# Performance work log

Measured on AMD Instinct MI355X. Metric: run time of the kernel, lower is better.

The kernel has to match this reference:

```python
import jax, jax.numpy as jnp
import numpy as np

BEAM = 10; MAX_LEN = 32; PAD = 1; BOS = 2; EOS = 3
NEG = jnp.float32(-1e30)


def lstm_cell(x, h, c, Wih, Whh, bih, bhh):
    # PyTorch LSTMCell gate order: i, f, g, o
    gates = x @ Wih.T + bih + h @ Whh.T + bhh
    i, f, g, o = jnp.split(gates, 4, axis=-1)
    c2 = jax.nn.sigmoid(f) * c + jax.nn.sigmoid(i) * jnp.tanh(g)
    h2 = jax.nn.sigmoid(o) * jnp.tanh(c2)
    return h2, c2


def setup_inputs() -> dict:
    key = jax.random.key(0)
    ks = jax.random.split(key, 14)
    G, P, E, H, S = 1000, 50000, 500, 500, 32
    s = lambda k, shape: jax.random.normal(k, shape, jnp.float32) * 0.05
    return {
        "g_seq": jax.random.randint(ks[0], (S, 1), 0, G),
        "enc_emb": s(ks[1], (G, E)),
        "enc_Wih": s(ks[2], (4 * H, E)), "enc_Whh": s(ks[3], (4 * H, H)),
        "enc_bih": s(ks[4], (4 * H,)), "enc_bhh": s(ks[5], (4 * H,)),
        "dec_emb": s(ks[6], (P, E)),
        "dec_Wih": s(ks[7], (4 * H, E)), "dec_Whh": s(ks[8], (4 * H, H)),
        "dec_bih": s(ks[9], (4 * H,)), "dec_bhh": s(ks[10], (4 * H,)),
        "attn_W": s(ks[11], (H, 2 * H)),
        "out_W": s(ks[12], (P, H)),
        "out_b": s(ks[13], (P,)),
    }


def reference(g_seq, enc_emb, enc_Wih, enc_Whh, enc_bih, enc_bhh,
              dec_emb, dec_Wih, dec_Whh, dec_bih, dec_bhh,
              attn_W, out_W, out_b):
    S = g_seq.shape[0]
    H = enc_Whh.shape[1]
    P = out_W.shape[0]

    # ---- encoder: unidirectional LSTMCell over seq, batch = 1 ----
    e_seq = enc_emb[g_seq[:, 0]]  # (S, E)
    def enc_step(carry, e):
        h, c = carry
        h, c = lstm_cell(e[None, :], h, c, enc_Wih, enc_Whh, enc_bih, enc_bhh)
        return (h, c), h[0]
    h0 = jnp.zeros((1, H), jnp.float32)
    (h, c), outs = jax.lax.scan(enc_step, (h0, h0), e_seq)  # outs: (S, H)

    # expand encoder state / context to beam
    context = jnp.broadcast_to(outs[None, :, :], (BEAM, S, H))
    h = jnp.broadcast_to(h, (BEAM, H))
    c = jnp.broadcast_to(c, (BEAM, H))
    scores = jnp.zeros((BEAM,), jnp.float32)
    tokens = jnp.full((BEAM,), PAD, jnp.int32).at[0].set(BOS)
    row0 = (jnp.arange(BEAM)[:, None] == 0)  # first-step mask: only beam 0 valid

    # ---- beam-search decode loop (run full max_len; early-eos break omitted,
    #      see notes: with eos=3 it only changes output when eos tops beam 0) ----
    def dec_step(carry, t):
        h, c, scores, tokens = carry
        e = dec_emb[tokens]                                   # (BEAM, E)
        h2, c2 = lstm_cell(e, h, c, dec_Wih, dec_Whh, dec_bih, dec_bhh)
        # dot attention
        attn = jax.nn.softmax(jnp.einsum('bsh,bh->bs', context, h2), axis=1)
        wctx = jnp.einsum('bs,bsh->bh', attn, context)
        o = jnp.tanh(jnp.concatenate([h2, wctx], axis=1) @ attn_W.T)
        logp = jax.nn.log_softmax(o @ out_W.T + out_b, axis=1)  # (BEAM, P)
        # first step: only beam 0 participates (original uses workd_lk[0])
        beam_lk = jnp.where(t == 0,
                            jnp.where(row0, logp, NEG),
                            logp + scores[:, None])
        best, idx = jax.lax.top_k(beam_lk.reshape(-1), BEAM)
        prev_k = idx // P
        next_y = idx - prev_k * P
        return (h2[prev_k], c2[prev_k], best, next_y), (prev_k, next_y)

    (_, _, scores, _), (prevKs, nextYs) = jax.lax.scan(
        dec_step, (h, c, scores, tokens), jnp.arange(MAX_LEN))

    # ---- hypothesis traceback, vectorized over beams ----
    def tb_step(k, t):
        tok = nextYs[t][k]
        return prevKs[t][k], tok
    _, toks = jax.lax.scan(tb_step, jnp.arange(BEAM), jnp.arange(MAX_LEN - 1, -1, -1))
    hyps = toks[::-1].T  # (BEAM, MAX_LEN)
    return hyps
```

## Files before the change

### kernel.cpp

```cpp
#include <hip/hip_runtime.h>
#include <math.h>

#define BEAM   10
#define MAXLEN 32
#define SLEN   32
#define HD     500
#define ED     500
#define G4     2000
#define PV     50000
#define NEGF   (-1e30f)

#define OFF_X      0
#define OFF_CBUF   64000
#define OFF_GBUF   65000
#define OFF_CTX    69000
#define OFF_DH     85000
#define OFF_DC     90000
#define OFF_DG     95000
#define OFF_H2     115000
#define OFF_C2     120000
#define OFF_WCTX   125000
#define OFF_O      130000
#define OFF_SCD    135000
#define OFF_TOK    135020
#define OFF_PREVK  135040
#define OFF_NEXTY  135360
#define OFF_PARTD  136000
#define OFF_CAND   152000
#define OFF_LOG    160000
#define OFF_OWT    660000
#define NEED_T_BYTES ((size_t)(OFF_OWT + (size_t)HD * PV) * 4)

__device__ __forceinline__ float sigf(float x) { return 1.f / (1.f + expf(-x)); }

__device__ __forceinline__ unsigned fkey(float f) {
    unsigned u = __float_as_uint(f);
    return (u & 0x80000000u) ? ~u : (u | 0x80000000u);
}
__device__ __forceinline__ float unfkey(unsigned k) {
    unsigned u = (k & 0x80000000u) ? (k & 0x7fffffffu) : ~k;
    return __uint_as_float(u);
}

__global__ void k_prep(const int* __restrict__ g_seq, const float* __restrict__ enc_emb,
                       const float* __restrict__ Wih, const float* __restrict__ bih,
                       const float* __restrict__ bhh, float* __restrict__ X,
                       float* __restrict__ cbuf0) {
    if (blockIdx.x == 0) {
        for (int j = threadIdx.x; j < HD; j += 256) cbuf0[j] = 0.f;
    }
    int wv = (blockIdx.x * blockDim.x + threadIdx.x) >> 6;
    int lane = threadIdx.x & 63;
    if (wv >= SLEN * G4) return;
    int t = wv / G4, r = wv - t * G4;
    const float* emb = enc_emb + (size_t)g_seq[t] * ED;
    const float* w = Wih + (size_t)r * ED;
    float acc = 0.f;
    for (int ki = 0; ki < 8; ki++) { int k = ki * 64 + lane; if (k < ED) acc += emb[k] * w[k]; }
    for (int o = 32; o; o >>= 1) acc += __shfl_down(acc, o);
    if (lane == 0) X[t * G4 + r] = acc + bih[r] + bhh[r];
}

__global__ void k_transpose(const float* __restrict__ outW, float* __restrict__ outWT) {
    __shared__ float t_lds[64][65];
    int tid = threadIdx.x;
    int pbase = blockIdx.x * 64, kbase = blockIdx.y * 64;
    for (int e = 0; e < 16; e++) {
        int idx = e * 256 + tid; int pl = idx >> 6, kl = idx & 63;
        int pp = pbase + pl, kk = kbase + kl;
        t_lds[pl][kl] = (pp < PV && kk < HD) ? outW[(size_t)pp * HD + kk] : 0.f;
    }
    __syncthreads();
    for (int e = 0; e < 16; e++) {
        int idx = e * 256 + tid; int kl = idx >> 6, pl = idx & 63;
        int pp = pbase + pl, kk = kbase + kl;
        if (pp < PV && kk < HD) outWT[(size_t)kk * PV + pp] = t_lds[pl][kl];
    }
}

__global__ void k_enc(const float* __restrict__ Whh, const float* __restrict__ X,
                      float* __restrict__ gbuf, float* __restrict__ cbuf,
                      float* __restrict__ context, float* __restrict__ dec_h,
                      float* __restrict__ dec_c, double* __restrict__ scores,
                      int* __restrict__ tokens, int t) {
    __shared__ float h_lds[HD];
    const float* gprev = gbuf + ((t + 1) & 1) * G4;
    float*       gcur  = gbuf + (t & 1) * G4;
    const float* cprev = cbuf + ((t + 1) & 1) * HD;
    float*       ccur  = cbuf + (t & 1) * HD;
    int tid = threadIdx.x;
    if (t > 0) {
        for (int j = tid; j < HD; j += 256) {
            float gi = gprev[j], gf = gprev[HD + j], gg = gprev[2 * HD + j], go = gprev[3 * HD + j];
            float c = sigf(gf) * cprev[j] + sigf(gi) * tanhf(gg);
            float h = sigf(go) * tanhf(c);
            h_lds[j] = h;
            if (blockIdx.x == 0) {
                ccur[j] = c;
                context[(t - 1) * HD + j] = h;
                if (t == SLEN) {
                    for (int b = 0; b < BEAM; b++) { dec_h[b * HD + j] = h; dec_c[b * HD + j] = c; }
                }
            }
        }
    } else {
        for (int j = tid; j < HD; j += 256) h_lds[j] = 0.f;
    }
    if (t == SLEN && blockIdx.x == 0 && tid == 0) {
        for (int b = 0; b < BEAM; b++) scores[b] = 0.0;
        tokens[0] = 2; for (int b = 1; b < BEAM; b++) tokens[b] = 1;
    }
    __syncthreads();
    if (t < SLEN) {
        int wv = blockIdx.x * 4 + (tid >> 6), lane = tid & 63;
        for (int r = wv; r < G4; r += 1000) {
            const float* w = Whh + (size_t)r * HD;
            float acc = 0.f;
            for (int ki = 0; ki < 8; ki++) { int k = ki * 64 + lane; if (k < HD) acc += h_lds[k] * w[k]; }
            for (int o = 32; o; o >>= 1) acc += __shfl_down(acc, o);
            if (lane == 0) gcur[r] = X[t * G4 + r] + acc;
        }
    }
}

__global__ __launch_bounds__(1024) void k_gates(
        const float* __restrict__ dec_emb, const float* __restrict__ Wih,
        const float* __restrict__ Whh, const float* __restrict__ bih,
        const float* __restrict__ bhh, const int* __restrict__ tokens,
        const float* __restrict__ h_ws, float* __restrict__ gates) {
    __shared__ float e_lds[BEAM * ED];
    __shared__ float h_lds[BEAM * HD];
    int tid = threadIdx.x;
    for (int idx = tid; idx < BEAM * ED; idx += 1024) {
        int b = idx / ED, k = idx - b * ED;
        e_lds[idx] = dec_emb[(size_t)tokens[b] * ED + k];
        h_lds[idx] = h_ws[idx];
    }
    __syncthreads();
    int wv = tid >> 6, lane = tid & 63;
    int r = blockIdx.x * 16 + wv;
    const float* wi = Wih + (size_t)r * ED;
    const float* wh = Whh + (size_t)r * HD;
    float acc[BEAM];
#pragma unroll
    for (int b = 0; b < BEAM; b++) acc[b] = 0.f;
    for (int ki = 0; ki < 8; ki++) {
        int k = ki * 64 + lane;
        if (k < ED) {
            float w = wi[k];
#pragma unroll
            for (int b = 0; b < BEAM; b++) acc[b] += w * e_lds[b * ED + k];
        }
    }
    for (int ki = 0; ki < 8; ki++) {
        int k = ki * 64 + lane;
        if (k < HD) {
            float w = wh[k];
#pragma unroll
            for (int b = 0; b < BEAM; b++) acc[b] += w * h_lds[b * HD + k];
        }
    }
#pragma unroll
    for (int b = 0; b < BEAM; b++) {
        float v = acc[b];
        for (int o = 32; o; o >>= 1) v += __shfl_down(v, o);
        acc[b] = v;
    }
    if (lane == 0) {
        float bb = bih[r] + bhh[r];
#pragma unroll
        for (int b = 0; b < BEAM; b++) gates[b * G4 + r] = acc[b] + bb;
    }
}

__global__ void k_attn(const float* __restrict__ gates, const float* __restrict__ c_ws,
                       const float* __restrict__ context, float* __restrict__ h2_ws,
                       float* __restrict__ c2_ws, float* __restrict__ wctx_ws) {
    __shared__ float h2_lds[HD];
    __shared__ float s_lds[SLEN];
    __shared__ float a_lds[SLEN];
    int b = blockIdx.x, tid = threadIdx.x;
    for (int j = tid; j < HD; j += 256) {
        float gi = gates[b * G4 + j], gf = gates[b * G4 + HD + j];
        float gg = gates[b * G4 + 2 * HD + j], go = gates[b * G4 + 3 * HD + j];
        float c = sigf(gf) * c_ws[b * HD + j] + sigf(gi) * tanhf(gg);
        float h2 = sigf(go) * tanhf(c);
        c2_ws[b * HD + j] = c; h2_ws[b * HD + j] = h2; h2_lds[j] = h2;
    }
    __syncthreads();
    int wv = tid >> 6, lane = tid & 63;
    for (int s = wv; s < SLEN; s += 4) {
        const float* ctx = context + s * HD;
        float acc = 0.f;
        for (int ki = 0; ki < 8; ki++) { int k = ki * 64 + lane; if (k < HD) acc += ctx[k] * h2_lds[k]; }
        for (int o = 32; o; o >>= 1) acc += __shfl_down(acc, o);
        if (lane == 0) s_lds[s] = acc;
    }
    __syncthreads();
    if (wv == 0) {
        float v = (lane < SLEN) ? s_lds[lane] : -INFINITY;
        float m = v;
        for (int o = 32; o; o >>= 1) m = fmaxf(m, __shfl_xor(m, o));
        float e = (lane < SLEN) ? expf(v - m) : 0.f;
        float sum = e;
        for (int o = 32; o; o >>= 1) sum += __shfl_xor(sum, o);
        if (lane < SLEN) a_lds[lane] = e / sum;
    }
    __syncthreads();
    for (int j = tid; j < HD; j += 256) {
        float w = 0.f;
        for (int s = 0; s < SLEN; s++) w += a_lds[s] * context[s * HD + j];
        wctx_ws[b * HD + j] = w;
    }
}

__global__ void k_oproj(const float* __restrict__ attnW, const float* __restrict__ h2_ws,
                        const float* __restrict__ wctx_ws, float* __restrict__ o_ws) {
    __shared__ float hw[BEAM * 1000];
    int tid = threadIdx.x;
    for (int idx = tid; idx < BEAM * 1000; idx += 256) {
        int b = idx / 1000, k = idx - b * 1000;
        hw[idx] = (k < HD) ? h2_ws[b * HD + k] : wctx_ws[b * HD + k - HD];
    }
    __syncthreads();
    int wv = tid >> 6, lane = tid & 63;
    int j = blockIdx.x * 4 + wv;
    const float* w = attnW + (size_t)j * 1000;
    float acc[BEAM];
#pragma unroll
    for (int b = 0; b < BEAM; b++) acc[b] = 0.f;
    for (int ki = 0; ki < 16; ki++) {
        int k = ki * 64 + lane;
        if (k < 1000) {
            float wk = w[k];
#pragma unroll
            for (int b = 0; b < BEAM; b++) acc[b] += wk * hw[b * 1000 + k];
        }
    }
#pragma unroll
    for (int b = 0; b < BEAM; b++) {
        float v = acc[b];
        for (int o = 32; o; o >>= 1) v += __shfl_down(v, o);
        acc[b] = v;
    }
    if (lane == 0) {
#pragma unroll
        for (int b = 0; b < BEAM; b++) o_ws[b * HD + j] = tanhf(acc[b]);
    }
}

__global__ void k_logits_t(const float* __restrict__ outWT, const float* __restrict__ outB,
                           const float* __restrict__ o_ws, float* __restrict__ logits,
                           double* __restrict__ partials) {
    __shared__ __align__(16) float o_kb[HD * 12];
    __shared__ double redd[256];
    int tid = threadIdx.x;
    for (int idx = tid; idx < BEAM * HD; idx += 256) {
        int b = idx / HD, k = idx - b * HD;
        o_kb[k * 12 + b] = o_ws[idx];
    }
    __syncthreads();
    int p = blockIdx.x * 256 + tid;
    bool valid = (p < PV);
    int pc = valid ? p : (PV - 1);
    float acc[BEAM];
#pragma unroll
    for (int b = 0; b < BEAM; b++) acc[b] = 0.f;
    for (int k = 0; k < HD; k++) {
        float w = outWT[(size_t)k * PV + pc];
        const float4* o4 = (const float4*)&o_kb[k * 12];
        float4 a = o4[0], b4 = o4[1];
        float2 c2 = *(const float2*)&o_kb[k * 12 + 8];
        acc[0] += w * a.x;  acc[1] += w * a.y;  acc[2] += w * a.z;  acc[3] += w * a.w;
        acc[4] += w * b4.x; acc[5] += w * b4.y; acc[6] += w * b4.z; acc[7] += w * b4.w;
        acc[8] += w * c2.x; acc[9] += w * c2.y;
    }
    float ob = outB[pc];
    double eacc[BEAM];
#pragma unroll
    for (int b = 0; b < BEAM; b++) {
        float lg = acc[b] + ob;
        if (valid) logits[(size_t)b * PV + p] = lg;
        eacc[b] = valid ? exp((double)lg) : 0.0;
    }
#pragma unroll
    for (int b = 0; b < BEAM; b++) {
        __syncthreads();
        redd[tid] = eacc[b];
        __syncthreads();
        for (int s = 128; s; s >>= 1) { if (tid < s) redd[tid] += redd[tid + s]; __syncthreads(); }
        if (tid == 0) partials[blockIdx.x * BEAM + b] = redd[0];
    }
}

__global__ void k_logits_f(const float* __restrict__ outW, const float* __restrict__ outB,
                           const float* __restrict__ o_ws, float* __restrict__ logits,
                           double* __restrict__ partials) {
    __shared__ float o_lds[BEAM * HD];
    __shared__ double ered[4][BEAM];
    int tid = threadIdx.x;
    for (int idx = tid; idx < BEAM * HD; idx += 256) o_lds[idx] = o_ws[idx];
    __syncthreads();
    int wv = tid >> 6, lane = tid & 63;
    int w = blockIdx.x * 4 + wv;
    double esum = 0.0;
    for (int pi = 0; pi < 16; pi++) {
        int p = w * 16 + pi;
        if (p >= PV) break;
        const float* wr = outW + (size_t)p * HD;
        float acc[BEAM];
#pragma unroll
        for (int b = 0; b < BEAM; b++) acc[b] = 0.f;
        for (int ki = 0; ki < 8; ki++) {
            int k = ki * 64 + lane;
            if (k < HD) {
                float x = wr[k];
#pragma unroll
                for (int b = 0; b < BEAM; b++) acc[b] += x * o_lds[b * HD + k];
            }
        }
#pragma unroll
        for (int b = 0; b < BEAM; b++)
            for (int o = 32; o; o >>= 1) acc[b] += __shfl_xor(acc[b], o);
        if (lane < BEAM) {
            float lg = 0.f;
#pragma unroll
            for (int b = 0; b < BEAM; b++) if (lane == b) lg = acc[b];
            lg += outB[p];
            logits[(size_t)lane * PV + p] = lg;
            esum += exp((double)lg);
        }
    }
    if (lane < BEAM) ered[wv][lane] = esum;
    __syncthreads();
    if (tid < BEAM) partials[blockIdx.x * BEAM + tid] =
        ered[0][tid] + ered[1][tid] + ered[2][tid] + ered[3][tid];
}

__global__ void k_topk_row(const float* __restrict__ logits, unsigned long long* __restrict__ cands) {
    const int CH = 1563;
    int r = blockIdx.x >> 5, ci = blockIdx.x & 31;
    int base = ci * CH;
    int tid = threadIdx.x;
    unsigned long long key[7];
#pragma unroll
    for (int e = 0; e < 7; e++) {
        int p = base + e * 256 + tid;
        key[e] = 0ull;
        if (p < base + CH && p < PV) {
            float v = logits[(size_t)r * PV + p];
            key[e] = ((unsigned long long)fkey(v) << 32) | (unsigned)(~(unsigned)p);
        }
    }
    __shared__ unsigned long long m[256];
    for (int round = 0; round < BEAM; round++) {
        unsigned long long mx = 0ull;
#pragma unroll
        for (int e = 0; e < 7; e++) if (key[e] > mx) mx = key[e];
        m[tid] = mx;
        __syncthreads();
        for (int s = 128; s; s >>= 1) {
            if (tid < s && m[tid + s] > m[tid]) m[tid] = m[tid + s];
            __syncthreads();
        }
        unsigned long long win = m[0];
        __syncthreads();
#pragma unroll
        for (int e = 0; e < 7; e++) if (key[e] == win) key[e] = 0ull;
        if (tid == 0) cands[blockIdx.x * BEAM + round] = win;
    }
}

__global__ void k_merge(const double* __restrict__ partials, int npart,
                        const unsigned long long* __restrict__ cands,
                        double* __restrict__ scores, int* __restrict__ tokens,
                        const float* __restrict__ h2_ws, const float* __restrict__ c2_ws,
                        float* __restrict__ h_ws, float* __restrict__ c_ws,
                        int* __restrict__ prevKs, int* __restrict__ nextYs, int t) {
    __shared__ double redd[256];
    __shared__ double lse_lds[BEAM];
    __shared__ double sc_lds[BEAM];
    __shared__ double mv[256];
    __shared__ unsigned mf[256];
    __shared__ int pk_lds[BEAM];
    __shared__ int ny_lds[BEAM];
    __shared__ double val_lds[BEAM];
    int tid = threadIdx.x;
    if (tid < BEAM) sc_lds[tid] = scores[tid];
    for (int b = 0; b < BEAM; b++) {
        double s = 0.0;
        for (int j = tid; j < npart; j += 256) s += partials[j * BEAM + b];
        redd[tid] = s;
        __syncthreads();
        for (int st = 128; st; st >>= 1) { if (tid < st) redd[tid] += redd[tid + st]; __syncthreads(); }
        if (tid == 0) lse_lds[b] = log(redd[0]);
        __syncthreads();
    }
    double   cv[13];
    unsigned cf[13];
#pragma unroll
    for (int e = 0; e < 13; e++) {
        int c = e * 256 + tid;
        cv[e] = -1.0e308; cf[e] = 0xFFFFFFFFu;
        if (c < 3200) {
            unsigned long long k0 = cands[c];
            if (k0) {
                int r = c / 320;
                float v = unfkey((unsigned)(k0 >> 32));
                unsigned p = ~((unsigned)k0);
                double v2;
                if (t == 0) v2 = (r == 0) ? ((double)v - lse_lds[0]) : (double)NEGF;
                else        v2 = ((double)v - lse_lds[r]) + sc_lds[r];
                cv[e] = v2;
                cf[e] = (unsigned)r * PV + p;
            }
        }
    }
    for (int round = 0; round < BEAM; round++) {
        double bv = -1.0e308; unsigned bf = 0xFFFFFFFFu;
#pragma unroll
        for (int e = 0; e < 13; e++) {
            if (cv[e] > bv || (cv[e] == bv && cf[e] < bf)) { bv = cv[e]; bf = cf[e]; }
        }
        mv[tid] = bv; mf[tid] = bf;
        __syncthreads();
        for (int s = 128; s; s >>= 1) {
            if (tid < s) {
                if (mv[tid + s] > mv[tid] || (mv[tid + s] == mv[tid] && mf[tid + s] < mf[tid])) {
                    mv[tid] = mv[tid + s]; mf[tid] = mf[tid + s];
                }
            }
            __syncthreads();
        }
        double wvv = mv[0]; unsigned wff = mf[0];
        __syncthreads();
#pragma unroll
        for (int e = 0; e < 13; e++) {
            if (cf[e] == wff) { cv[e] = -1.0e308; cf[e] = 0xFFFFFFFFu; }
        }
        if (tid == 0) {
            int pk = (int)(wff / PV);
            int ny = (int)(wff - (unsigned)pk * PV);
            pk_lds[round] = pk; ny_lds[round] = ny; val_lds[round] = wvv;
        }
        __syncthreads();
    }
    if (tid < BEAM) {
        scores[tid] = val_lds[tid];
        tokens[tid] = ny_lds[tid];
        prevKs[t * BEAM + tid] = pk_lds[tid];
        nextYs[t * BEAM + tid] = ny_lds[tid];
    }
    __syncthreads();
    for (int idx = tid; idx < BEAM * HD; idx += 256) {
        int i = idx / HD, j = idx - i * HD;
        h_ws[idx] = h2_ws[pk_lds[i] * HD + j];
        c_ws[idx] = c2_ws[pk_lds[i] * HD + j];
    }
}

__global__ void k_traceback(const int* __restrict__ prevKs, const int* __restrict__ nextYs,
                            int* __restrict__ out) {
    int k = threadIdx.x;
    if (k >= BEAM) return;
    int cur = k;
    for (int t = MAXLEN - 1; t >= 0; t--) {
        out[k * MAXLEN + t] = nextYs[t * BEAM + cur];
        cur = prevKs[t * BEAM + cur];
    }
}

extern "C" void kernel_launch(void* const* d_in, const int* in_sizes, int n_in,
                              void* d_out, int out_size, void* d_ws, size_t ws_size,
                              hipStream_t stream) {
    const int*   g_seq  = (const int*)  d_in[0];
    const float* encEmb = (const float*)d_in[1];
    const float* encWih = (const float*)d_in[2];
    const float* encWhh = (const float*)d_in[3];
    const float* encBih = (const float*)d_in[4];
    const float* encBhh = (const float*)d_in[5];
    const float* decEmb = (const float*)d_in[6];
    const float* decWih = (const float*)d_in[7];
    const float* decWhh = (const float*)d_in[8];
    const float* decBih = (const float*)d_in[9];
    const float* decBhh = (const float*)d_in[10];
    const float* attnW  = (const float*)d_in[11];
    const float* outW   = (const float*)d_in[12];
    const float* outB   = (const float*)d_in[13];

    float* ws = (float*)d_ws;
    float*  X     = ws + OFF_X;
    float*  cbuf  = ws + OFF_CBUF;
    float*  gbuf  = ws + OFF_GBUF;
    float*  ctx   = ws + OFF_CTX;
    float*  dh    = ws + OFF_DH;
    float*  dc    = ws + OFF_DC;
    float*  dg    = ws + OFF_DG;
    float*  h2    = ws + OFF_H2;
    float*  c2    = ws + OFF_C2;
    float*  wctx  = ws + OFF_WCTX;
    float*  o     = ws + OFF_O;
    double* sc    = (double*)(ws + OFF_SCD);
    int*    tok   = (int*)(ws + OFF_TOK);
    int*    prevK = (int*)(ws + OFF_PREVK);
    int*    nextY = (int*)(ws + OFF_NEXTY);
    double* part  = (double*)(ws + OFF_PARTD);
    unsigned long long* cand = (unsigned long long*)(ws + OFF_CAND);
    float*  logits = ws + OFF_LOG;
    float*  outWT  = ws + OFF_OWT;

    bool bigws = (ws_size >= NEED_T_BYTES);

    k_prep<<<16000, 256, 0, stream>>>(g_seq, encEmb, encWih, encBih, encBhh, X, cbuf);
    if (bigws) k_transpose<<<dim3(782, 8), 256, 0, stream>>>(outW, outWT);

    for (int t = 0; t <= SLEN; t++)
        k_enc<<<250, 256, 0, stream>>>(encWhh, X, gbuf, cbuf, ctx, dh, dc, sc, tok, t);

    int npart = bigws ? 196 : 782;
    for (int t = 0; t < MAXLEN; t++) {
        k_gates<<<125, 1024, 0, stream>>>(decEmb, decWih, decWhh, decBih, decBhh, tok, dh, dg);
        k_attn<<<BEAM, 256, 0, stream>>>(dg, dc, ctx, h2, c2, wctx);
        k_oproj<<<125, 256, 0, stream>>>(attnW, h2, wctx, o);
        if (bigws) k_logits_t<<<196, 256, 0, stream>>>(outWT, outB, o, logits, part);
        else       k_logits_f<<<782, 256, 0, stream>>>(outW, outB, o, logits, part);
        k_topk_row<<<320, 256, 0, stream>>>(logits, cand);
        k_merge<<<1, 256, 0, stream>>>(part, npart, cand, sc, tok, h2, c2, dh, dc, prevK, nextY, t);
    }
    k_traceback<<<1, 64, 0, stream>>>(prevK, nextY, (int*)d_out);
}
```

Measured before the change: 4.370 ms.

## Fuse attention with output projection, use float4 k-blocked logits, and use wave-level reductions

Attention and the attn_W projection are merged into one kernel. Each of the 125 blocks recomputes the LSTM cell, the attention scores and the weighted context for all beams in LDS, which removes a launch and the wctx round trip through global memory. The transposed out_W is stored in 4-wide k blocks, and the logits kernel now splits K across waves in 782 blocks, giving more parallelism and float4 loads. Top-k and merge replace shared-memory tree reductions with wave shuffles, which cuts barriers. The cost is attention work repeated 125 times per step and more LDS per block.

```diff
diff --git a/kernel.cpp b/kernel.cpp
--- a/kernel.cpp
+++ b/kernel.cpp
@@ -19,7 +19,6 @@
 #define OFF_DG     95000
 #define OFF_H2     115000
 #define OFF_C2     120000
-#define OFF_WCTX   125000
 #define OFF_O      130000
 #define OFF_SCD    135000
 #define OFF_TOK    135020
@@ -31,6 +30,8 @@
 #define OFF_OWT    660000
 #define NEED_T_BYTES ((size_t)(OFF_OWT + (size_t)HD * PV) * 4)
 
+typedef unsigned long long u64;
+
 __device__ __forceinline__ float sigf(float x) { return 1.f / (1.f + expf(-x)); }
 
 __device__ __forceinline__ unsigned fkey(float f) {
@@ -61,7 +62,7 @@
     if (lane == 0) X[t * G4 + r] = acc + bih[r] + bhh[r];
 }
 
-__global__ void k_transpose(const float* __restrict__ outW, float* __restrict__ outWT) {
+__global__ void k_transpose4(const float* __restrict__ outW, float* __restrict__ outW4) {
     __shared__ float t_lds[64][65];
     int tid = threadIdx.x;
     int pbase = blockIdx.x * 64, kbase = blockIdx.y * 64;
@@ -71,10 +72,19 @@
         t_lds[pl][kl] = (pp < PV && kk < HD) ? outW[(size_t)pp * HD + kk] : 0.f;
     }
     __syncthreads();
-    for (int e = 0; e < 16; e++) {
-        int idx = e * 256 + tid; int kl = idx >> 6, pl = idx & 63;
-        int pp = pbase + pl, kk = kbase + kl;
-        if (pp < PV && kk < HD) outWT[(size_t)kk * PV + pp] = t_lds[pl][kl];
+    for (int e = 0; e < 4; e++) {
+        int idx = e * 256 + tid;
+        int pl = idx & 63, kb = idx >> 6;
+        int pp = pbase + pl;
+        int kglob = kbase + kb * 4;
+        if (pp < PV && kglob < HD) {
+            float4 v;
+            v.x = t_lds[pl][kb * 4 + 0];
+            v.y = t_lds[pl][kb * 4 + 1];
+            v.z = t_lds[pl][kb * 4 + 2];
+            v.w = t_lds[pl][kb * 4 + 3];
+            *(float4*)(outW4 + ((size_t)(kbase / 4 + kb) * PV + pp) * 4) = v;
+        }
     }
 }
 
@@ -173,57 +183,80 @@
     }
 }
 
-__global__ void k_attn(const float* __restrict__ gates, const float* __restrict__ c_ws,
-                       const float* __restrict__ context, float* __restrict__ h2_ws,
-                       float* __restrict__ c2_ws, float* __restrict__ wctx_ws) {
-    __shared__ float h2_lds[HD];
-    __shared__ float s_lds[SLEN];
-    __shared__ float a_lds[SLEN];
-    int b = blockIdx.x, tid = threadIdx.x;
-    for (int j = tid; j < HD; j += 256) {
+__global__ __launch_bounds__(256) void k_attn_oproj(
+        const float* __restrict__ gates, const float* __restrict__ c_ws,
+        const float* __restrict__ context, const float* __restrict__ attnW,
+        float* __restrict__ h2_ws, float* __restrict__ c2_ws, float* __restrict__ o_ws) {
+    __shared__ float h2_lds[BEAM * HD];
+    __shared__ float wctx_lds[BEAM * HD];
+    __shared__ float s_lds[BEAM * SLEN];
+    __shared__ float a_lds[BEAM * SLEN];
+    int tid = threadIdx.x;
+    int wv = tid >> 6, lane = tid & 63;
+    for (int idx = tid; idx < BEAM * HD; idx += 256) {
+        int b = idx / HD, j = idx - b * HD;
         float gi = gates[b * G4 + j], gf = gates[b * G4 + HD + j];
         float gg = gates[b * G4 + 2 * HD + j], go = gates[b * G4 + 3 * HD + j];
-        float c = sigf(gf) * c_ws[b * HD + j] + sigf(gi) * tanhf(gg);
+        float c = sigf(gf) * c_ws[idx] + sigf(gi) * tanhf(gg);
         float h2 = sigf(go) * tanhf(c);
-        c2_ws[b * HD + j] = c; h2_ws[b * HD + j] = h2; h2_lds[j] = h2;
-    }
-    __syncthreads();
-    int wv = tid >> 6, lane = tid & 63;
-    for (int s = wv; s < SLEN; s += 4) {
-        const float* ctx = context + s * HD;
-        float acc = 0.f;
-        for (int ki = 0; ki < 8; ki++) { int k = ki * 64 + lane; if (k < HD) acc += ctx[k] * h2_lds[k]; }
-        for (int o = 32; o; o >>= 1) acc += __shfl_down(acc, o);
-        if (lane == 0) s_lds[s] = acc;
+        h2_lds[idx] = h2;
+        if (blockIdx.x == 0) { c2_ws[idx] = c; h2_ws[idx] = h2; }
+    }
+    __syncthreads();
+    for (int si = 0; si < 8; ++si) {
+        int s = wv + 4 * si;
+        float acc[BEAM];
+#pragma unroll
+        for (int b = 0; b < BEAM; b++) acc[b] = 0.f;
+        for (int ki = 0; ki < 8; ki++) {
+            int k = ki * 64 + lane;
+            if (k < HD) {
+                float c = context[s * HD + k];
+#pragma unroll
+                for (int b = 0; b < BEAM; b++) acc[b] += c * h2_lds[b * HD + k];
+            }
+        }
+#pragma unroll
+        for (int b = 0; b < BEAM; b++) {
+            float v = acc[b];
+            for (int o = 32; o; o >>= 1) v += __shfl_down(v, o);
+            if (lane == 0) s_lds[b * SLEN + s] = v;
+        }
     }
     __syncthreads();
     if (wv == 0) {
-        float v = (lane < SLEN) ? s_lds[lane] : -INFINITY;
-        float m = v;
-        for (int o = 32; o; o >>= 1) m = fmaxf(m, __shfl_xor(m, o));
-        float e = (lane < SLEN) ? expf(v - m) : 0.f;
-        float sum = e;
-        for (int o = 32; o; o >>= 1) sum += __shfl_xor(sum, o);
-        if (lane < SLEN) a_lds[lane] = e / sum;
-    }
-    __syncthreads();
-    for (int j = tid; j < HD; j += 256) {
-        float w = 0.f;
-        for (int s = 0; s < SLEN; s++) w += a_lds[s] * context[s * HD + j];
-        wctx_ws[b * HD + j] = w;
-    }
-}
-
-__global__ void k_oproj(const float* __restrict__ attnW, const float* __restrict__ h2_ws,
-                        const float* __restrict__ wctx_ws, float* __restrict__ o_ws) {
-    __shared__ float hw[BEAM * 1000];
-    int tid = threadIdx.x;
-    for (int idx = tid; idx < BEAM * 1000; idx += 256) {
-        int b = idx / 1000, k = idx - b * 1000;
-        hw[idx] = (k < HD) ? h2_ws[b * HD + k] : wctx_ws[b * HD + k - HD];
-    }
-    __syncthreads();
-    int wv = tid >> 6, lane = tid & 63;
+        for (int b = 0; b < BEAM; ++b) {
+            float v = (lane < SLEN) ? s_lds[b * SLEN + lane] : -INFINITY;
+            float m = v;
+            for (int o = 32; o; o >>= 1) m = fmaxf(m, __shfl_xor(m, o));
+            float e = (lane < SLEN) ? expf(v - m) : 0.f;
+            float sum = e;
+            for (int o = 32; o; o >>= 1) sum += __shfl_xor(sum, o);
+            if (lane < SLEN) a_lds[b * SLEN + lane] = e / sum;
+        }
+    }
+    __syncthreads();
+    {
+        float w0[BEAM], w1[BEAM];
+#pragma unroll
+        for (int b = 0; b < BEAM; b++) { w0[b] = 0.f; w1[b] = 0.f; }
+        int j0 = tid, j1 = tid + 256;
+        for (int s = 0; s < SLEN; ++s) {
+            float c0 = (j0 < HD) ? context[s * HD + j0] : 0.f;
+            float c1 = (j1 < HD) ? context[s * HD + j1] : 0.f;
+#pragma unroll
+            for (int b = 0; b < BEAM; b++) {
+                float a = a_lds[b * SLEN + s];
+                w0[b] += a * c0; w1[b] += a * c1;
+            }
+        }
+#pragma unroll
+        for (int b = 0; b < BEAM; b++) {
+            if (j0 < HD) wctx_lds[b * HD + j0] = w0[b];
+            if (j1 < HD) wctx_lds[b * HD + j1] = w1[b];
+        }
+    }
+    __syncthreads();
     int j = blockIdx.x * 4 + wv;
     const float* w = attnW + (size_t)j * 1000;
     float acc[BEAM];
@@ -234,7 +267,10 @@
         if (k < 1000) {
             float wk = w[k];
 #pragma unroll
-            for (int b = 0; b < BEAM; b++) acc[b] += wk * hw[b * 1000 + k];
+            for (int b = 0; b < BEAM; b++) {
+                float h = (k < HD) ? h2_lds[b * HD + k] : wctx_lds[b * HD + k - HD];
+                acc[b] += wk * h;
+            }
         }
     }
 #pragma unroll
@@ -249,47 +285,56 @@
     }
 }
 
-__global__ void k_logits_t(const float* __restrict__ outWT, const float* __restrict__ outB,
-                           const float* __restrict__ o_ws, float* __restrict__ logits,
-                           double* __restrict__ partials) {
-    __shared__ __align__(16) float o_kb[HD * 12];
-    __shared__ double redd[256];
-    int tid = threadIdx.x;
-    for (int idx = tid; idx < BEAM * HD; idx += 256) {
-        int b = idx / HD, k = idx - b * HD;
-        o_kb[k * 12 + b] = o_ws[idx];
-    }
-    __syncthreads();
-    int p = blockIdx.x * 256 + tid;
-    bool valid = (p < PV);
-    int pc = valid ? p : (PV - 1);
+__global__ __launch_bounds__(256) void k_logits4(
+        const float* __restrict__ outW4, const float* __restrict__ outB,
+        const float* __restrict__ o_ws, float* __restrict__ logits,
+        double* __restrict__ partials) {
+    __shared__ __align__(16) float4 o4[BEAM * 125];
+    __shared__ float part[4][64][BEAM];
+    int tid = threadIdx.x;
+    for (int idx = tid; idx < BEAM * 125; idx += 256) {
+        int b = idx / 125, kb = idx - b * 125;
+        o4[idx] = *(const float4*)(o_ws + b * HD + kb * 4);
+    }
+    __syncthreads();
+    int kc = tid >> 6, pl = tid & 63;
+    int p = blockIdx.x * 64 + pl;
+    int pc = (p < PV) ? p : (PV - 1);
+    int kb0 = kc * 32, kb1 = (kc == 3) ? 125 : (kb0 + 32);
     float acc[BEAM];
 #pragma unroll
     for (int b = 0; b < BEAM; b++) acc[b] = 0.f;
-    for (int k = 0; k < HD; k++) {
-        float w = outWT[(size_t)k * PV + pc];
-        const float4* o4 = (const float4*)&o_kb[k * 12];
-        float4 a = o4[0], b4 = o4[1];
-        float2 c2 = *(const float2*)&o_kb[k * 12 + 8];
-        acc[0] += w * a.x;  acc[1] += w * a.y;  acc[2] += w * a.z;  acc[3] += w * a.w;
-        acc[4] += w * b4.x; acc[5] += w * b4.y; acc[6] += w * b4.z; acc[7] += w * b4.w;
-        acc[8] += w * c2.x; acc[9] += w * c2.y;
-    }
-    float ob = outB[pc];
-    double eacc[BEAM];
-#pragma unroll
-    for (int b = 0; b < BEAM; b++) {
-        float lg = acc[b] + ob;
-        if (valid) logits[(size_t)b * PV + p] = lg;
-        eacc[b] = valid ? exp((double)lg) : 0.0;
-    }
-#pragma unroll
-    for (int b = 0; b < BEAM; b++) {
-        __syncthreads();
-        redd[tid] = eacc[b];
-        __syncthreads();
-        for (int s = 128; s; s >>= 1) { if (tid < s) redd[tid] += redd[tid + s]; __syncthreads(); }
-        if (tid == 0) partials[blockIdx.x * BEAM + b] = redd[0];
+    const float4* wp = (const float4*)outW4;
+    for (int kb = kb0; kb < kb1; ++kb) {
+        float4 w = wp[(size_t)kb * PV + pc];
+#pragma unroll
+        for (int b = 0; b < BEAM; b++) {
+            float4 o = o4[b * 125 + kb];
+            acc[b] += w.x * o.x + w.y * o.y + w.z * o.z + w.w * o.w;
+        }
+    }
+#pragma unroll
+    for (int b = 0; b < BEAM; b++) part[kc][pl][b] = acc[b];
+    __syncthreads();
+    if (tid < 64) {
+        int p2 = blockIdx.x * 64 + tid;
+        bool valid = (p2 < PV);
+        float ob = outB[valid ? p2 : 0];
+        double es[BEAM];
+#pragma unroll
+        for (int b = 0; b < BEAM; b++) {
+            float lg = part[0][tid][b] + part[1][tid][b] + part[2][tid][b] + part[3][tid][b] + ob;
+            if (valid) logits[(size_t)b * PV + p2] = lg;
+            es[b] = valid ? exp((double)lg) : 0.0;
+        }
+#pragma unroll
+        for (int b = 0; b < BEAM; b++) {
+            for (int o = 32; o; o >>= 1) es[b] += __shfl_down(es[b], o);
+        }
+        if (tid == 0) {
+#pragma unroll
+            for (int b = 0; b < BEAM; b++) partials[blockIdx.x * BEAM + b] = es[b];
+        }
     }
 }
 
@@ -337,63 +382,75 @@
         ered[0][tid] + ered[1][tid] + ered[2][tid] + ered[3][tid];
 }
 
-__global__ void k_topk_row(const float* __restrict__ logits, unsigned long long* __restrict__ cands) {
+__global__ __launch_bounds__(256) void k_topk_row(const float* __restrict__ logits,
+                                                  u64* __restrict__ cands) {
     const int CH = 1563;
     int r = blockIdx.x >> 5, ci = blockIdx.x & 31;
     int base = ci * CH;
     int tid = threadIdx.x;
-    unsigned long long key[7];
+    int wv = tid >> 6, lane = tid & 63;
+    u64 key[7];
 #pragma unroll
     for (int e = 0; e < 7; e++) {
         int p = base + e * 256 + tid;
         key[e] = 0ull;
         if (p < base + CH && p < PV) {
             float v = logits[(size_t)r * PV + p];
-            key[e] = ((unsigned long long)fkey(v) << 32) | (unsigned)(~(unsigned)p);
-        }
-    }
-    __shared__ unsigned long long m[256];
+            key[e] = ((u64)fkey(v) << 32) | (unsigned)(~(unsigned)p);
+        }
+    }
+    __shared__ u64 wred[4];
+    __shared__ u64 winlds;
     for (int round = 0; round < BEAM; round++) {
-        unsigned long long mx = 0ull;
+        u64 mx = 0ull;
 #pragma unroll
         for (int e = 0; e < 7; e++) if (key[e] > mx) mx = key[e];
-        m[tid] = mx;
+        for (int o = 32; o; o >>= 1) {
+            u64 other = __shfl_down(mx, o);
+            if (other > mx) mx = other;
+        }
+        if (lane == 0) wred[wv] = mx;
         __syncthreads();
-        for (int s = 128; s; s >>= 1) {
-            if (tid < s && m[tid + s] > m[tid]) m[tid] = m[tid + s];
-            __syncthreads();
-        }
-        unsigned long long win = m[0];
+        if (tid == 0) {
+            u64 wn = wred[0];
+            for (int i = 1; i < 4; i++) if (wred[i] > wn) wn = wred[i];
+            winlds = wn;
+            cands[blockIdx.x * BEAM + round] = wn;
+        }
         __syncthreads();
+        u64 win = winlds;
 #pragma unroll
         for (int e = 0; e < 7; e++) if (key[e] == win) key[e] = 0ull;
-        if (tid == 0) cands[blockIdx.x * BEAM + round] = win;
-    }
-}
-
-__global__ void k_merge(const double* __restrict__ partials, int npart,
-                        const unsigned long long* __restrict__ cands,
-                        double* __restrict__ scores, int* __restrict__ tokens,
-                        const float* __restrict__ h2_ws, const float* __restrict__ c2_ws,
-                        float* __restrict__ h_ws, float* __restrict__ c_ws,
-                        int* __restrict__ prevKs, int* __restrict__ nextYs, int t) {
-    __shared__ double redd[256];
+    }
+}
+
+__global__ __launch_bounds__(256) void k_merge(
+        const double* __restrict__ partials, int npart,
+        const u64* __restrict__ cands,
+        double* __restrict__ scores, int* __restrict__ tokens,
+        const float* __restrict__ h2_ws, const float* __restrict__ c2_ws,
+        float* __restrict__ h_ws, float* __restrict__ c_ws,
+        int* __restrict__ prevKs, int* __restrict__ nextYs, int t) {
+    __shared__ double wredd[4];
     __shared__ double lse_lds[BEAM];
     __shared__ double sc_lds[BEAM];
-    __shared__ double mv[256];
-    __shared__ unsigned mf[256];
+    __shared__ double bwv[4];
+    __shared__ unsigned bwf[4];
+    __shared__ double winv_s;
+    __shared__ unsigned winf_s;
     __shared__ int pk_lds[BEAM];
     __shared__ int ny_lds[BEAM];
     __shared__ double val_lds[BEAM];
     int tid = threadIdx.x;
+    int wv = tid >> 6, lane = tid & 63;
     if (tid < BEAM) sc_lds[tid] = scores[tid];
     for (int b = 0; b < BEAM; b++) {
         double s = 0.0;
         for (int j = tid; j < npart; j += 256) s += partials[j * BEAM + b];
-        redd[tid] = s;
+        for (int o = 32; o; o >>= 1) s += __shfl_down(s, o);
+        if (lane == 0) wredd[wv] = s;
         __syncthreads();
-        for (int st = 128; st; st >>= 1) { if (tid < st) redd[tid] += redd[tid + st]; __syncthreads(); }
-        if (tid == 0) lse_lds[b] = log(redd[0]);
+        if (tid == 0) lse_lds[b] = log(wredd[0] + wredd[1] + wredd[2] + wredd[3]);
         __syncthreads();
     }
     double   cv[13];
@@ -403,7 +460,7 @@
         int c = e * 256 + tid;
         cv[e] = -1.0e308; cf[e] = 0xFFFFFFFFu;
         if (c < 3200) {
-            unsigned long long k0 = cands[c];
+            u64 k0 = cands[c];
             if (k0) {
                 int r = c / 320;
                 float v = unfkey((unsigned)(k0 >> 32));
@@ -422,28 +479,29 @@
         for (int e = 0; e < 13; e++) {
             if (cv[e] > bv || (cv[e] == bv && cf[e] < bf)) { bv = cv[e]; bf = cf[e]; }
         }
-        mv[tid] = bv; mf[tid] = bf;
+        for (int o = 32; o; o >>= 1) {
+            double ov = __shfl_down(bv, o);
+            unsigned of = __shfl_down(bf, o);
+            if (ov > bv || (ov == bv && of < bf)) { bv = ov; bf = of; }
+        }
+        if (lane == 0) { bwv[wv] = bv; bwf[wv] = bf; }
         __syncthreads();
-        for (int s = 128; s; s >>= 1) {
-            if (tid < s) {
-                if (mv[tid + s] > mv[tid] || (mv[tid + s] == mv[tid] && mf[tid + s] < mf[tid])) {
-                    mv[tid] = mv[tid + s]; mf[tid] = mf[tid + s];
-                }
-            }
-            __syncthreads();
-        }
-        double wvv = mv[0]; unsigned wff = mf[0];
+        if (tid == 0) {
+            double xv = bwv[0]; unsigned xf = bwf[0];
+            for (int i = 1; i < 4; i++) {
+                if (bwv[i] > xv || (bwv[i] == xv && bwf[i] < xf)) { xv = bwv[i]; xf = bwf[i]; }
+            }
+            winv_s = xv; winf_s = xf;
+            int pk = (int)(xf / PV);
+            int ny = (int)(xf - (unsigned)pk * PV);
+            pk_lds[round] = pk; ny_lds[round] = ny; val_lds[round] = xv;
+        }
         __syncthreads();
+        unsigned wff = winf_s;
 #pragma unroll
         for (int e = 0; e < 13; e++) {
             if (cf[e] == wff) { cv[e] = -1.0e308; cf[e] = 0xFFFFFFFFu; }
         }
-        if (tid == 0) {
-            int pk = (int)(wff / PV);
-            int ny = (int)(wff - (unsigned)pk * PV);
-            pk_lds[round] = pk; ny_lds[round] = ny; val_lds[round] = wvv;
-        }
-        __syncthreads();
     }
     if (tid < BEAM) {
         scores[tid] = val_lds[tid];
@@ -498,31 +556,29 @@
     float*  dg    = ws + OFF_DG;
     float*  h2    = ws + OFF_H2;
     float*  c2    = ws + OFF_C2;
-    float*  wctx  = ws + OFF_WCTX;
     float*  o     = ws + OFF_O;
     double* sc    = (double*)(ws + OFF_SCD);
     int*    tok   = (int*)(ws + OFF_TOK);
     int*    prevK = (int*)(ws + OFF_PREVK);
     int*    nextY = (int*)(ws + OFF_NEXTY);
     double* part  = (double*)(ws + OFF_PARTD);
-    unsigned long long* cand = (unsigned long long*)(ws + OFF_CAND);
+    u64*    cand  = (u64*)(ws + OFF_CAND);
     float*  logits = ws + OFF_LOG;
-    float*  outWT  = ws + OFF_OWT;
+    float*  outW4  = ws + OFF_OWT;
 
     bool bigws = (ws_size >= NEED_T_BYTES);
 
     k_prep<<<16000, 256, 0, stream>>>(g_seq, encEmb, encWih, encBih, encBhh, X, cbuf);
-    if (bigws) k_transpose<<<dim3(782, 8), 256, 0, stream>>>(outW, outWT);
+    if (bigws) k_transpose4<<<dim3(782, 8), 256, 0, stream>>>(outW, outW4);
 
     for (int t = 0; t <= SLEN; t++)
         k_enc<<<250, 256, 0, stream>>>(encWhh, X, gbuf, cbuf, ctx, dh, dc, sc, tok, t);
 
-    int npart = bigws ? 196 : 782;
+    const int npart = 782;
     for (int t = 0; t < MAXLEN; t++) {
         k_gates<<<125, 1024, 0, stream>>>(decEmb, decWih, decWhh, decBih, decBhh, tok, dh, dg);
-        k_attn<<<BEAM, 256, 0, stream>>>(dg, dc, ctx, h2, c2, wctx);
-        k_oproj<<<125, 256, 0, stream>>>(attnW, h2, wctx, o);
-        if (bigws) k_logits_t<<<196, 256, 0, stream>>>(outWT, outB, o, logits, part);
+        k_attn_oproj<<<125, 256, 0, stream>>>(dg, dc, ctx, attnW, h2, c2, o);
+        if (bigws) k_logits4<<<782, 256, 0, stream>>>(outW4, outB, o, logits, part);
         else       k_logits_f<<<782, 256, 0, stream>>>(outW, outB, o, logits, part);
         k_topk_row<<<320, 256, 0, stream>>>(logits, cand);
         k_merge<<<1, 256, 0, stream>>>(part, npart, cand, sc, tok, h2, c2, dh, dc, prevK, nextY, t);
```

Result: faster. 4.218 ms (-3.5%).
